# Kernel tuning notes

Measured on AMD Instinct MI355X. Metric: run time of the kernel, lower is better.

The kernel has to match this reference:

```python
import jax, jax.numpy as jnp
import numpy as np

B, IMG_ROWS, TSTEPS = 64, 32, 128
HID, CIN = 64, 512  # ncde hidden, ncde input dim = 32 * (IMG_ROWS//2)


def _linear(x, w, b):
    return x @ w.T + b


def _conv(x, w, b, pad):
    y = jax.lax.conv_general_dilated(x, w, (1, 1), [(pad, pad), (pad, pad)],
                                     dimension_numbers=('NCHW', 'OIHW', 'NCHW'))
    return y + b[None, :, None, None]


def _maxpool2(x):
    return jax.lax.reduce_window(x, -jnp.inf, jax.lax.max, (1, 1, 2, 2), (1, 1, 2, 2), 'VALID')


def _natural_cubic_coeffs(x):
    # x: [B, L, C], uniform knots t=0..L-1 (h=1). Natural cubic spline.
    L = x.shape[1]
    n = L - 2
    A = 4.0 * jnp.eye(n, dtype=x.dtype) + jnp.eye(n, k=1, dtype=x.dtype) + jnp.eye(n, k=-1, dtype=x.dtype)
    rhs = 6.0 * (x[:, 2:] - 2.0 * x[:, 1:-1] + x[:, :-2])  # [B, n, C]
    Mi = jnp.linalg.solve(A, rhs.transpose(1, 0, 2).reshape(n, -1))
    Mi = Mi.reshape(n, x.shape[0], x.shape[2]).transpose(1, 0, 2)
    M = jnp.pad(Mi, ((0, 0), (1, 1), (0, 0)))  # natural BCs: M0 = M_{L-1} = 0
    a = x[:, :-1]
    b = (x[:, 1:] - x[:, :-1]) - (2.0 * M[:, :-1] + M[:, 1:]) / 6.0
    c = M[:, :-1] / 2.0
    d = (M[:, 1:] - M[:, :-1]) / 6.0
    return a, b, c, d  # each [B, L-1, C]


def _forward(x, conv1_w, conv1_b, conv2_w, conv2_b, att_fc1_w, att_fc1_b,
             att_fc2_w, att_fc2_b, initial_w, initial_b, f1_w, f1_b,
             f2_w, f2_b, out_w, out_b):
    h = jax.nn.relu(_conv(x, conv1_w, conv1_b, pad=2))
    h = jax.nn.relu(_conv(h, conv2_w, conv2_b, pad=1))
    h = _maxpool2(h)  # [B,32,16,T/2]  (dropout is identity in eval)
    att = h.mean(axis=(2, 3))  # AdaptiveAvgPool2d(1)
    att = jax.nn.sigmoid(_linear(jax.nn.relu(_linear(att, att_fc1_w, att_fc1_b)), att_fc2_w, att_fc2_b))
    h = h * att[:, :, None, None]
    h = jnp.transpose(h, (0, 3, 1, 2))
    seq = h.reshape(h.shape[0], h.shape[1], -1)  # [B, L, 512]
    L = seq.shape[1]
    _, sb, sc, sd = _natural_cubic_coeffs(seq)

    z0 = _linear(seq[:, 0], initial_w, initial_b)  # spline.evaluate(t0) == seq[:,0]

    def cdefunc(z):
        u = jax.nn.relu(_linear(z, f1_w, f1_b))
        u = jnp.tanh(_linear(u, f2_w, f2_b))
        return u.reshape(z.shape[0], HID, CIN)

    def dXdt(t):
        seg = jnp.clip(jnp.floor(t).astype(jnp.int32), 0, L - 2)
        fr = t - seg.astype(t.dtype)
        return sb[:, seg] + 2.0 * sc[:, seg] * fr + 3.0 * sd[:, seg] * fr * fr

    def vf(t, z):
        return jnp.einsum('bhc,bc->bh', cdefunc(z), dXdt(t))

    dt = jnp.float32(0.5)
    nsteps = 2 * (L - 1)

    @jax.checkpoint
    def step(z, t):
        k1 = vf(t, z)
        k2 = vf(t + dt / 2, z + dt / 2 * k1)
        k3 = vf(t + dt / 2, z + dt / 2 * k2)
        k4 = vf(t + dt, z + dt * k3)
        return z + dt / 6.0 * (k1 + 2 * k2 + 2 * k3 + k4), None

    ts = jnp.arange(nsteps, dtype=jnp.float32) * dt
    zT, _ = jax.lax.scan(step, z0, ts)
    return _linear(zT, out_w, out_b)


def setup_inputs() -> dict:
    key = jax.random.key(0)
    ks = jax.random.split(key, 10)
    s = lambda k, shape, sc=0.05: (jax.random.normal(k, shape, jnp.float32) * sc)
    z = lambda n: jnp.zeros((n,), jnp.float32)
    return {
        'x': jax.random.normal(ks[0], (B, 1, IMG_ROWS, TSTEPS), jnp.float32),
        'conv1_w': s(ks[1], (32, 1, 5, 5)), 'conv1_b': z(32),
        'conv2_w': s(ks[2], (32, 32, 3, 3)), 'conv2_b': z(32),
        'att_fc1_w': s(ks[3], (4, 32)), 'att_fc1_b': z(4),
        'att_fc2_w': s(ks[4], (32, 4)), 'att_fc2_b': z(32),
        'initial_w': s(ks[5], (HID, CIN)), 'initial_b': z(HID),
        'f1_w': s(ks[6], (128, HID)), 'f1_b': z(128),
        'f2_w': s(ks[7], (CIN * HID, 128)), 'f2_b': z(CIN * HID),
        'out_w': s(ks[8], (2, HID)), 'out_b': z(2),
    }


def reference(x, conv1_w, conv1_b, conv2_w, conv2_b, att_fc1_w, att_fc1_b,
              att_fc2_w, att_fc2_b, initial_w, initial_b, f1_w, f1_b,
              f2_w, f2_b, out_w, out_b):
    return _forward(x, conv1_w, conv1_b, conv2_w, conv2_b, att_fc1_w, att_fc1_b,
                    att_fc2_w, att_fc2_b, initial_w, initial_b, f1_w, f1_b,
                    f2_w, f2_b, out_w, out_b)
```

## Files before the change

kernel.cpp:

```cpp
#include <hip/hip_runtime.h>
#include <hip/hip_bf16.h>
#include <stdint.h>

#define NSTEP 126
#define NEVAL 504
#define POISON 0xAAAAAAAAu

typedef __bf16 v8bf __attribute__((ext_vector_type(8)));
typedef float  v4f  __attribute__((ext_vector_type(4)));

__device__ __forceinline__ unsigned short f2bf(float x) {
  union { float f; uint32_t u; } v; v.f = x;
  uint32_t u = v.u;
  uint32_t r = (u + 0x7FFFu + ((u >> 16) & 1u)) >> 16;
  return (unsigned short)r;
}
__device__ __forceinline__ float bf2f(unsigned short b) {
  union { uint32_t u; float f; } v; v.u = ((uint32_t)b) << 16;
  return v.f;
}

__global__ void k_detect(const uint32_t* __restrict__ xw, int* flag) {
  __shared__ int cnt;
  if (threadIdx.x == 0) cnt = 0;
  __syncthreads();
  uint32_t w = xw[threadIdx.x];
  int e = (int)((w >> 7) & 0xFF);
  int good = ((e >= 100) && (e <= 144)) || ((w & 0xFFFFu) == 0u);
  atomicAdd(&cnt, good);
  __syncthreads();
  if (threadIdx.x == 0) *flag = (cnt >= 192) ? 1 : 0;
}

#define NCVT 15
struct CvtArgs {
  const void* src[NCVT];
  int dstoff[NCVT];
  int len[NCVT];
  int kind[NCVT];
  int total;
};
__global__ void k_convert(CvtArgs a, float* __restrict__ ws, const int* __restrict__ flag) {
  int f = *flag;
  for (int i = blockIdx.x*256 + threadIdx.x; i < a.total; i += gridDim.x*256) {
    int t = 0; int rem = i;
    while (rem >= a.len[t]) { rem -= a.len[t]; t++; }
    float v = f ? bf2f(((const unsigned short*)a.src[t])[rem])
                : ((const float*)a.src[t])[rem];
    int d;
    if (a.kind[t] == 1) { int h = rem >> 9, c = rem & 511; d = a.dstoff[t] + c*64 + h; }
    else if (a.kind[t] == 2) {
      int co = rem / 288, r2 = rem % 288;
      int ci = r2 / 9, tt = r2 % 9;
      d = a.dstoff[t] + (co >> 4)*4608 + (ci*16 + (co & 15))*9 + tt;
    }
    else d = a.dstoff[t] + rem;
    ws[d] = v;
  }
}

__global__ void k_wbf16(const void* __restrict__ w2src, const void* __restrict__ w1src,
                        unsigned short* __restrict__ w2bf, unsigned short* __restrict__ w1bf,
                        const int* __restrict__ flag) {
  int f = *flag;
  const long N2 = 4194304, N1 = 8192;
  for (long i = (long)blockIdx.x*256 + threadIdx.x; i < N2 + N1; i += (long)gridDim.x*256) {
    if (i < N2) w2bf[i] = f ? ((const unsigned short*)w2src)[i] : f2bf(((const float*)w2src)[i]);
    else { long j = i - N2; w1bf[j] = f ? ((const unsigned short*)w1src)[j] : f2bf(((const float*)w1src)[j]); }
  }
}

__global__ void k_conv1(const float* __restrict__ xf, const float* __restrict__ w,
                        const float* __restrict__ bias, float* __restrict__ h1) {
  int x = threadIdx.x;
  int y = blockIdx.x;
  int b = blockIdx.y;
  const float* xin = xf + (long)b*4096;
  float in[25];
  #pragma unroll
  for (int ky = 0; ky < 5; ky++) {
    int yy = y + ky - 2;
    #pragma unroll
    for (int kx = 0; kx < 5; kx++) {
      int xx = x + kx - 2;
      in[ky*5+kx] = (yy >= 0 && yy < 32 && xx >= 0 && xx < 128) ? xin[yy*128 + xx] : 0.f;
    }
  }
  for (int co = 0; co < 32; co++) {
    float acc = bias[co];
    #pragma unroll
    for (int t = 0; t < 25; t++) acc += in[t] * w[co*25 + t];
    h1[(((long)b*32 + co)*32 + y)*128 + x] = fmaxf(acc, 0.f);
  }
}

#define LD2 132
__global__ __launch_bounds__(256) void k_conv2(const float* __restrict__ h1, const float* __restrict__ w,
                                               const float* __restrict__ bias, float* __restrict__ h2) {
  __shared__ float s[32][3][LD2];
  int y = blockIdx.x, b = blockIdx.y;
  int tid = threadIdx.x;
  for (int i = tid; i < 32*3*LD2; i += 256) {
    int ci = i / (3*LD2);
    int r  = (i / LD2) % 3;
    int xx = i % LD2;
    int yy = y + r - 1, sx = xx - 1;
    float v = 0.f;
    if (yy >= 0 && yy < 32 && sx >= 0 && sx < 128) v = h1[(((long)b*32+ci)*32+yy)*128+sx];
    s[ci][r][xx] = v;
  }
  __syncthreads();
  int x = tid & 127;
  int half = __builtin_amdgcn_readfirstlane(tid >> 7);
  const float* wb = w + half*4608;
  float acc[16];
  #pragma unroll
  for (int i = 0; i < 16; i++) acc[i] = bias[half*16 + i];
  #pragma unroll 2
  for (int ci = 0; ci < 32; ci++) {
    float xv[9];
    #pragma unroll
    for (int r = 0; r < 3; r++)
      #pragma unroll
      for (int k = 0; k < 3; k++) xv[r*3+k] = s[ci][r][x + k];
    #pragma unroll
    for (int co = 0; co < 16; co++) {
      const float* wr = wb + (ci*16 + co)*9;
      #pragma unroll
      for (int t = 0; t < 9; t++) acc[co] += xv[t] * wr[t];
    }
  }
  #pragma unroll
  for (int co = 0; co < 16; co++)
    h2[(((long)b*32 + half*16 + co)*32 + y)*128 + x] = fmaxf(acc[co], 0.f);
}

__global__ void k_pool(const float* __restrict__ h2, float* __restrict__ pooled, float* __restrict__ attm) {
  int bc = blockIdx.x;
  const float* src = h2 + (long)bc*4096;
  float* dst = pooled + (long)bc*1024;
  float sum = 0.f;
  for (int i = threadIdx.x; i < 1024; i += 256) {
    int py = i >> 6, px = i & 63;
    const float* p = src + py*256 + px*2;
    float m = fmaxf(fmaxf(p[0], p[1]), fmaxf(p[128], p[129]));
    dst[i] = m;
    sum += m;
  }
  __shared__ float red[256];
  red[threadIdx.x] = sum;
  __syncthreads();
  for (int s2 = 128; s2 > 0; s2 >>= 1) {
    if (threadIdx.x < s2) red[threadIdx.x] += red[threadIdx.x + s2];
    __syncthreads();
  }
  if (threadIdx.x == 0) attm[bc] = red[0] * (1.f/1024.f);
}

__global__ void k_att(const float* __restrict__ attm, const float* __restrict__ w1, const float* __restrict__ b1,
                      const float* __restrict__ w2, const float* __restrict__ b2, float* __restrict__ atts) {
  int b = threadIdx.x;
  if (b < 64) {
    float hb[4];
    #pragma unroll
    for (int j = 0; j < 4; j++) {
      float s = b1[j];
      for (int i = 0; i < 32; i++) s += attm[b*32+i]*w1[j*32+i];
      hb[j] = fmaxf(s, 0.f);
    }
    for (int o = 0; o < 32; o++) {
      float s = b2[o];
      #pragma unroll
      for (int j = 0; j < 4; j++) s += hb[j]*w2[o*4+j];
      atts[b*32+o] = 1.f/(1.f + __expf(-s));
    }
  }
}

__global__ void k_seq(const float* __restrict__ pooled, const float* __restrict__ atts, float* __restrict__ seq) {
  for (int idx = blockIdx.x*256 + threadIdx.x; idx < 64*64*512; idx += gridDim.x*256) {
    int b = idx >> 15;
    int t = (idx >> 9) & 63;
    int fch = idx & 511;
    int c = fch >> 4, hh = fch & 15;
    seq[idx] = pooled[(((long)b*32 + c)*16 + hh)*64 + t] * atts[b*32 + c];
  }
}

__global__ __launch_bounds__(256, 1) void k_spline(const float* __restrict__ seq, float* __restrict__ sb,
                                                   float* __restrict__ sc, float* __restrict__ sd) {
  int id = blockIdx.x*256 + threadIdx.x;
  int b = id >> 9, f = id & 511;
  const float* xp = seq + (long)b*32768 + f;
  float xv[64];
  #pragma unroll
  for (int t = 0; t < 64; t++) xv[t] = xp[t*512];
  float cp[62], dp[62];
  float pc = 0.f, pd = 0.f;
  #pragma unroll
  for (int i = 0; i < 62; i++) {
    float rhs = 6.f*(xv[i+2] - 2.f*xv[i+1] + xv[i]);
    float inv = 1.f/(4.f - pc);
    pc = inv;
    pd = (rhs - pd)*inv;
    cp[i] = pc; dp[i] = pd;
  }
  #pragma unroll
  for (int i = 60; i >= 0; i--) dp[i] = dp[i] - cp[i]*dp[i+1];
  const float i6 = 1.f/6.f;
  #pragma unroll
  for (int t = 0; t < 63; t++) {
    float M0 = (t == 0)  ? 0.f : dp[t-1];
    float M1 = (t == 62) ? 0.f : dp[t];
    long o = ((long)b*63 + t)*512 + f;
    sb[o] = (xv[t+1] - xv[t]) - (2.f*M0 + M1)*i6;
    sc[o] = 0.5f*M0;
    sd[o] = (M1 - M0)*i6;
  }
}

__global__ void k_dxt(const float* __restrict__ sb, const float* __restrict__ sc,
                      const float* __restrict__ sd, float* __restrict__ dxt) {
  for (long i = (long)blockIdx.x*256 + threadIdx.x; i < (long)253*32768; i += (long)gridDim.x*256) {
    int m = (int)(i >> 15);
    int bf = (int)(i & 32767);
    int b = bf >> 9, c = bf & 511;
    int seg = m >> 2; if (seg > 62) seg = 62;
    float fr = 0.25f*(float)m - (float)seg;
    long o = ((long)b*63 + seg)*512 + c;
    dxt[i] = sb[o] + 2.f*fr*sc[o] + (3.f*fr*fr)*sd[o];
  }
}

__global__ void k_z0(const float* __restrict__ seq, const float* __restrict__ iwT,
                     const float* __restrict__ ib, float* __restrict__ z0) {
  __shared__ float s0[512];
  int b = blockIdx.x, h = threadIdx.x;
  for (int c = h; c < 512; c += 64) s0[c] = seq[(long)b*32768 + c];
  __syncthreads();
  float acc = ib[h];
  for (int c = 0; c < 512; c++) acc += s0[c]*iwT[c*64 + h];
  z0[b*64 + h] = acc;
}

__global__ __launch_bounds__(512, 2) void k_ode(
    const float* __restrict__ z0buf,
    const unsigned short* __restrict__ w2bf,
    const unsigned short* __restrict__ w1bf,
    const float* __restrict__ f1bias,
    const float* __restrict__ f2bias,
    const float* __restrict__ dxt,
    const float* __restrict__ outw,
    const float* __restrict__ outb,
    uint32_t* kpart,
    void* dout,
    const int* __restrict__ flag)
{
  __shared__ __align__(16) unsigned short zs[16*72];
  __shared__ __align__(16) unsigned short ub[16*136];
  __shared__ __align__(16) float dxs[16*524 + 10560];
  __shared__ float kred[128];

  int tid = threadIdx.x;
  int bl  = blockIdx.x;
  int hb  = bl >> 2;
  int bq  = bl & 3;
  int B0  = bq*16;
  int lane = tid & 63, wv = tid >> 6;
  int q = lane >> 4, ln = lane & 15;

  v8bf w2f[4][4];
  #pragma unroll
  for (int jt = 0; jt < 4; jt++)
    #pragma unroll
    for (int ks = 0; ks < 4; ks++) {
      long row = (long)hb*512 + wv*64 + jt*16 + ln;
      w2f[jt][ks] = *(const v8bf*)(w2bf + row*128 + ks*32 + q*8);
    }
  v8bf w1f[2];
  #pragma unroll
  for (int ks = 0; ks < 2; ks++)
    w1f[ks] = *(const v8bf*)(w1bf + (wv*16 + ln)*64 + ks*32 + q*8);
  float fb2[4][4];
  #pragma unroll
  for (int jt = 0; jt < 4; jt++)
    #pragma unroll
    for (int r = 0; r < 4; r++)
      fb2[jt][r] = f2bias[(long)hb*512 + wv*64 + jt*16 + q*4 + r];
  float fb1[4];
  #pragma unroll
  for (int r = 0; r < 4; r++)
    fb1[r] = f1bias[wv*16 + q*4 + r];

  int zbL = tid & 15;
  int hg  = tid >> 4;
  int h0  = hg*2;
  float z[2], zacc[2];
  #pragma unroll
  for (int i = 0; i < 2; i++) { z[i] = z0buf[(B0+zbL)*64 + h0 + i]; zacc[i] = 0.f; }

  const float dt6 = 0.5f/6.f;
  int e = 0;
  for (int step = 0; step < NSTEP; step++) {
    #pragma unroll 1
    for (int stage = 0; stage < 4; stage++, e++) {
      bool do_dx = (stage == 1) || (stage == 3) || (e == 0);
      int m = 2*step + ((stage + 1) >> 1);
      float4 dxr[4];
      if (do_dx) {
        #pragma unroll
        for (int i = 0; i < 4; i++) {
          int fi = i*512 + tid;
          int bb = fi >> 7, c4 = fi & 127;
          dxr[i] = *(const float4*)(dxt + (long)m*32768 + (B0+bb)*512 + c4*4);
        }
      }
      if (e > 0) {
        const uint32_t* kp = kpart + ((long)(e-1)*4 + bq)*1024;
        if (tid >= 64 && tid < 128) {
          const uint32_t* pp = kp + (tid - 64)*16;
          while (__hip_atomic_load(pp, __ATOMIC_RELAXED, __HIP_MEMORY_SCOPE_AGENT) == POISON)
            __builtin_amdgcn_s_sleep(1);
        }
        __syncthreads();
        float kv[2];
        #pragma unroll
        for (int i = 0; i < 2; i++) {
          const uint32_t* p = kp + (h0+i)*16 + zbL;
          uint32_t v = __hip_atomic_load(p, __ATOMIC_RELAXED, __HIP_MEMORY_SCOPE_AGENT);
          while (v == POISON) {
            __builtin_amdgcn_s_sleep(1);
            v = __hip_atomic_load(p, __ATOMIC_RELAXED, __HIP_MEMORY_SCOPE_AGENT);
          }
          kv[i] = __uint_as_float(v);
        }
        if (stage == 0) {
          uint32_t pk = 0;
          #pragma unroll
          for (int i = 0; i < 2; i++) {
            z[i] += dt6*(zacc[i] + kv[i]);
            zacc[i] = 0.f;
            pk |= ((uint32_t)f2bf(z[i])) << (16*i);
          }
          *(uint32_t*)(zs + zbL*72 + h0) = pk;
        } else {
          float wk = (stage == 1) ? 1.f : 2.f;
          float aa = (stage == 3) ? 0.5f : 0.25f;
          uint32_t pk = 0;
          #pragma unroll
          for (int i = 0; i < 2; i++) {
            zacc[i] += wk*kv[i];
            pk |= ((uint32_t)f2bf(z[i] + aa*kv[i])) << (16*i);
          }
          *(uint32_t*)(zs + zbL*72 + h0) = pk;
        }
      } else {
        uint32_t pk = ((uint32_t)f2bf(z[0])) | (((uint32_t)f2bf(z[1])) << 16);
        *(uint32_t*)(zs + zbL*72 + h0) = pk;
      }
      if (do_dx) {
        #pragma unroll
        for (int i = 0; i < 4; i++) {
          int fi = i*512 + tid;
          int bb = fi >> 7, c4 = fi & 127;
          *(float4*)(dxs + bb*524 + c4*4) = dxr[i];
        }
      }
      __syncthreads();
      v8bf zf[2];
      #pragma unroll
      for (int ks = 0; ks < 2; ks++)
        zf[ks] = *(const v8bf*)(zs + ln*72 + ks*32 + q*8);
      {
        v4f ua = (v4f){0.f, 0.f, 0.f, 0.f};
        #pragma unroll
        for (int ks = 0; ks < 2; ks++)
          ua = __builtin_amdgcn_mfma_f32_16x16x32_bf16(w1f[ks], zf[ks], ua, 0, 0, 0);
        ushort4 pk;
        pk.x = f2bf(fmaxf(ua[0] + fb1[0], 0.f));
        pk.y = f2bf(fmaxf(ua[1] + fb1[1], 0.f));
        pk.z = f2bf(fmaxf(ua[2] + fb1[2], 0.f));
        pk.w = f2bf(fmaxf(ua[3] + fb1[3], 0.f));
        *(ushort4*)(ub + ln*136 + wv*16 + q*4) = pk;
      }
      __syncthreads();
      v8bf uf[4];
      #pragma unroll
      for (int ks = 0; ks < 4; ks++)
        uf[ks] = *(const v8bf*)(ub + ln*136 + ks*32 + q*8);
      float ksum = 0.f;
      #pragma unroll
      for (int jt = 0; jt < 4; jt++) {
        v4f acc = (v4f){0.f, 0.f, 0.f, 0.f};
        #pragma unroll
        for (int ks = 0; ks < 4; ks++)
          acc = __builtin_amdgcn_mfma_f32_16x16x32_bf16(w2f[jt][ks], uf[ks], acc, 0, 0, 0);
        v4f dx4 = *(const v4f*)(dxs + ln*524 + wv*64 + jt*16 + q*4);
        #pragma unroll
        for (int r = 0; r < 4; r++) {
          float xv2 = acc[r] + fb2[jt][r];
          float ex = __expf(2.f*xv2);
          float th = 1.f - 2.f*__builtin_amdgcn_rcpf(ex + 1.f);
          ksum += th*dx4[r];
        }
      }
      ksum += __shfl_xor(ksum, 16, 64);
      ksum += __shfl_xor(ksum, 32, 64);
      if (lane < 16)
        kred[wv*16 + ln] = ksum;
      __syncthreads();
      if (tid < 16) {
        float v = 0.f;
        #pragma unroll
        for (int w = 0; w < 8; w++) v += kred[w*16 + tid];
        uint32_t uv = __float_as_uint(v);
        if (uv == POISON) uv ^= 1u;
        __hip_atomic_store(kpart + (((long)e*4 + bq)*64 + hb)*16 + tid, uv,
                           __ATOMIC_RELAXED, __HIP_MEMORY_SCOPE_AGENT);
      }
    }
  }
  if (hb == 0) {
    const uint32_t* kp = kpart + ((long)(NEVAL-1)*4 + bq)*1024;
    if (tid >= 64 && tid < 128) {
      const uint32_t* pp = kp + (tid - 64)*16;
      while (__hip_atomic_load(pp, __ATOMIC_RELAXED, __HIP_MEMORY_SCOPE_AGENT) == POISON)
        __builtin_amdgcn_s_sleep(1);
    }
    __syncthreads();
    {
      #pragma unroll
      for (int i = 0; i < 2; i++) {
        const uint32_t* p = kp + (h0+i)*16 + zbL;
        uint32_t v = __hip_atomic_load(p, __ATOMIC_RELAXED, __HIP_MEMORY_SCOPE_AGENT);
        while (v == POISON) {
          __builtin_amdgcn_s_sleep(1);
          v = __hip_atomic_load(p, __ATOMIC_RELAXED, __HIP_MEMORY_SCOPE_AGENT);
        }
        z[i] += dt6*(zacc[i] + __uint_as_float(v));
      }
    }
    float o0 = z[0]*outw[h0] + z[1]*outw[h0+1];
    float o1 = z[0]*outw[64+h0] + z[1]*outw[64+h0+1];
    __syncthreads();
    dxs[hg*32 + zbL*2 + 0] = o0;
    dxs[hg*32 + zbL*2 + 1] = o1;
    __syncthreads();
    if (tid < 32) {
      int bloc = tid >> 1, comp = tid & 1;
      float s = outb[comp];
      #pragma unroll
      for (int g = 0; g < 32; g++) s += dxs[g*32 + bloc*2 + comp];
      int b = B0 + bloc;
      if (*flag) ((unsigned short*)dout)[b*2 + comp] = f2bf(s);
      else       ((float*)dout)[b*2 + comp] = s;
    }
  }
}

extern "C" void kernel_launch(void* const* d_in, const int* in_sizes, int n_in,
                              void* d_out, int out_size, void* d_ws, size_t ws_size,
                              hipStream_t stream) {
  (void)in_sizes; (void)n_in; (void)out_size; (void)ws_size;
  float* ws = (float*)d_ws;
  size_t o = 0;
  auto alloc = [&](size_t n) { size_t r = o; o += (n + 63) & ~(size_t)63; return r; };
  size_t o_flag = alloc(64);
  size_t o_xf   = alloc(262144);
  size_t o_c1w  = alloc(800);
  size_t o_c1b  = alloc(32);
  size_t o_c2w  = alloc(9216);
  size_t o_c2b  = alloc(32);
  size_t o_a1w  = alloc(128);
  size_t o_a1b  = alloc(4);
  size_t o_a2w  = alloc(128);
  size_t o_a2b  = alloc(32);
  size_t o_iwT  = alloc(32768);
  size_t o_ib   = alloc(64);
  size_t o_f1b  = alloc(128);
  size_t o_f2b  = alloc(32768);
  size_t o_ow   = alloc(128);
  size_t o_ob   = alloc(2);
  size_t o_z0   = alloc(4096);
  size_t o_attm = alloc(2048);
  size_t o_atts = alloc(2048);
  size_t o_w1bf = alloc(4096);
  size_t o_w2bf = alloc(2097152);
  size_t o_h1   = alloc(8388608);
  size_t o_h2   = alloc(8388608);
  size_t o_kpart= alloc(4128768);
  size_t o_pool = o_h1;
  size_t o_seq  = o_h1 + 2097152;
  size_t o_dxt  = o_h1;
  size_t o_sb   = o_h2;
  size_t o_sc   = o_h2 + 2064384;
  size_t o_sd   = o_h2 + 4128768;

  int* flag = (int*)(ws + o_flag);

  hipLaunchKernelGGL(k_detect, dim3(1), dim3(256), 0, stream, (const uint32_t*)d_in[0], flag);

  CvtArgs ca;
  const int  si[NCVT]  = {0,1,2,3,4,5,6,7,8,9,10,12,14,15,16};
  const size_t dofs[NCVT] = {o_xf,o_c1w,o_c1b,o_c2w,o_c2b,o_a1w,o_a1b,o_a2w,o_a2b,o_iwT,o_ib,o_f1b,o_f2b,o_ow,o_ob};
  const int  ln[NCVT]  = {262144,800,32,9216,32,128,4,128,32,32768,64,128,32768,128,2};
  int tot = 0;
  for (int i = 0; i < NCVT; i++) {
    ca.src[i] = d_in[si[i]];
    ca.dstoff[i] = (int)dofs[i];
    ca.len[i] = ln[i];
    ca.kind[i] = (si[i] == 9) ? 1 : ((si[i] == 3) ? 2 : 0);
    tot += ln[i];
  }
  ca.total = tot;
  hipLaunchKernelGGL(k_convert, dim3(512), dim3(256), 0, stream, ca, ws, flag);
  hipLaunchKernelGGL(k_wbf16, dim3(2048), dim3(256), 0, stream, d_in[13], d_in[11],
                     (unsigned short*)(ws + o_w2bf), (unsigned short*)(ws + o_w1bf), flag);
  hipLaunchKernelGGL(k_conv1, dim3(32,64), dim3(128), 0, stream, ws+o_xf, ws+o_c1w, ws+o_c1b, ws+o_h1);
  hipLaunchKernelGGL(k_conv2, dim3(32,64), dim3(256), 0, stream, ws+o_h1, ws+o_c2w, ws+o_c2b, ws+o_h2);
  hipLaunchKernelGGL(k_pool, dim3(2048), dim3(256), 0, stream, ws+o_h2, ws+o_pool, ws+o_attm);
  hipLaunchKernelGGL(k_att, dim3(1), dim3(64), 0, stream, ws+o_attm, ws+o_a1w, ws+o_a1b, ws+o_a2w, ws+o_a2b, ws+o_atts);
  hipLaunchKernelGGL(k_seq, dim3(2048), dim3(256), 0, stream, ws+o_pool, ws+o_atts, ws+o_seq);
  hipLaunchKernelGGL(k_spline, dim3(128), dim3(256), 0, stream, ws+o_seq, ws+o_sb, ws+o_sc, ws+o_sd);
  hipLaunchKernelGGL(k_z0, dim3(64), dim3(64), 0, stream, ws+o_seq, ws+o_iwT, ws+o_ib, ws+o_z0);
  hipLaunchKernelGGL(k_dxt, dim3(4096), dim3(256), 0, stream, ws+o_sb, ws+o_sc, ws+o_sd, ws+o_dxt);

  hipLaunchKernelGGL(k_ode, dim3(256), dim3(512), 0, stream,
                     ws + o_z0,
                     (const unsigned short*)(ws + o_w2bf),
                     (const unsigned short*)(ws + o_w1bf),
                     ws + o_f1b, ws + o_f2b,
                     ws + o_dxt, ws + o_ow, ws + o_ob,
                     (uint32_t*)(ws + o_kpart),
                     d_out, (const int*)flag);
}
```

Measured before the change: 1.649 ms.

## Fuse spline dX/dt into spline kernel and stage k partials through LDS

The separate dX/dt kernel is removed: the spline kernel now writes dX/dt directly at the quarter-step sample points, so the sb/sc/sd intermediates never round-trip through global memory. In the ODE kernel, 256 threads poll the cross-block k partials in vectorised groups and stage them in LDS, replacing per-thread spinning atomic loads. Biases are folded into the MFMA accumulator initial values, bf16 packing uses the hardware pack-convert instruction, and the kred reduction layout is reordered. The added LDS buffer raises shared memory use per block, and the hardware conversion may round differently from the software round-to-nearest-even.

After: 1.704 ms. 1.03x slower.

```diff
diff --git a/kernel.cpp b/kernel.cpp
--- a/kernel.cpp
+++ b/kernel.cpp
@@ -18,6 +18,11 @@
 __device__ __forceinline__ float bf2f(unsigned short b) {
   union { uint32_t u; float f; } v; v.u = ((uint32_t)b) << 16;
   return v.f;
+}
+__device__ __forceinline__ uint32_t cvt_pk_bf16(float lo, float hi) {
+  uint32_t r;
+  asm("v_cvt_pk_bf16_f32 %0, %1, %2" : "=v"(r) : "v"(lo), "v"(hi));
+  return r;
 }
 
 __global__ void k_detect(const uint32_t* __restrict__ xw, int* flag) {
@@ -187,8 +192,8 @@
   }
 }
 
-__global__ __launch_bounds__(256, 1) void k_spline(const float* __restrict__ seq, float* __restrict__ sb,
-                                                   float* __restrict__ sc, float* __restrict__ sd) {
+__global__ __launch_bounds__(256, 1) void k_spline(const float* __restrict__ seq,
+                                                   float* __restrict__ dxt) {
   int id = blockIdx.x*256 + threadIdx.x;
   int b = id >> 9, f = id & 511;
   const float* xp = seq + (long)b*32768 + f;
@@ -208,27 +213,20 @@
   #pragma unroll
   for (int i = 60; i >= 0; i--) dp[i] = dp[i] - cp[i]*dp[i+1];
   const float i6 = 1.f/6.f;
+  float* op = dxt + (long)b*512 + f;
   #pragma unroll
   for (int t = 0; t < 63; t++) {
     float M0 = (t == 0)  ? 0.f : dp[t-1];
     float M1 = (t == 62) ? 0.f : dp[t];
-    long o = ((long)b*63 + t)*512 + f;
-    sb[o] = (xv[t+1] - xv[t]) - (2.f*M0 + M1)*i6;
-    sc[o] = 0.5f*M0;
-    sd[o] = (M1 - M0)*i6;
-  }
-}
-
-__global__ void k_dxt(const float* __restrict__ sb, const float* __restrict__ sc,
-                      const float* __restrict__ sd, float* __restrict__ dxt) {
-  for (long i = (long)blockIdx.x*256 + threadIdx.x; i < (long)253*32768; i += (long)gridDim.x*256) {
-    int m = (int)(i >> 15);
-    int bf = (int)(i & 32767);
-    int b = bf >> 9, c = bf & 511;
-    int seg = m >> 2; if (seg > 62) seg = 62;
-    float fr = 0.25f*(float)m - (float)seg;
-    long o = ((long)b*63 + seg)*512 + c;
-    dxt[i] = sb[o] + 2.f*fr*sc[o] + (3.f*fr*fr)*sd[o];
+    float sb = (xv[t+1] - xv[t]) - (2.f*M0 + M1)*i6;
+    float sc = 0.5f*M0;
+    float sd = (M1 - M0)*i6;
+    float* o = op + (long)(4*t)*32768;
+    o[0]      = sb;
+    o[32768]  = sb + 0.5f*sc + 0.1875f*sd;
+    o[65536]  = sb + sc + 0.75f*sd;
+    o[98304]  = sb + 1.5f*sc + 1.6875f*sd;
+    if (t == 62) o[131072] = sb + 2.f*sc + 3.f*sd;
   }
 }
 
@@ -258,7 +256,8 @@
 {
   __shared__ __align__(16) unsigned short zs[16*72];
   __shared__ __align__(16) unsigned short ub[16*136];
-  __shared__ __align__(16) float dxs[16*524 + 10560];
+  __shared__ __align__(16) float dxs[16*524 + 9600];
+  __shared__ __align__(16) uint32_t klds[1024];
   __shared__ float kred[128];
 
   int tid = threadIdx.x;
@@ -317,53 +316,56 @@
       }
       if (e > 0) {
         const uint32_t* kp = kpart + ((long)(e-1)*4 + bq)*1024;
-        if (tid >= 64 && tid < 128) {
-          const uint32_t* pp = kp + (tid - 64)*16;
-          while (__hip_atomic_load(pp, __ATOMIC_RELAXED, __HIP_MEMORY_SCOPE_AGENT) == POISON)
-            __builtin_amdgcn_s_sleep(1);
+        if (tid >= 64 && tid < 320) {
+          int pt = tid - 64;
+          const uint32_t* pp = kp + pt*4;
+          uint32_t v0 = __hip_atomic_load(pp+0, __ATOMIC_RELAXED, __HIP_MEMORY_SCOPE_AGENT);
+          uint32_t v1 = __hip_atomic_load(pp+1, __ATOMIC_RELAXED, __HIP_MEMORY_SCOPE_AGENT);
+          uint32_t v2 = __hip_atomic_load(pp+2, __ATOMIC_RELAXED, __HIP_MEMORY_SCOPE_AGENT);
+          uint32_t v3 = __hip_atomic_load(pp+3, __ATOMIC_RELAXED, __HIP_MEMORY_SCOPE_AGENT);
+          while (v0 == POISON) { __builtin_amdgcn_s_sleep(1);
+            v0 = __hip_atomic_load(pp+0, __ATOMIC_RELAXED, __HIP_MEMORY_SCOPE_AGENT); }
+          while (v1 == POISON) { __builtin_amdgcn_s_sleep(1);
+            v1 = __hip_atomic_load(pp+1, __ATOMIC_RELAXED, __HIP_MEMORY_SCOPE_AGENT); }
+          while (v2 == POISON) { __builtin_amdgcn_s_sleep(1);
+            v2 = __hip_atomic_load(pp+2, __ATOMIC_RELAXED, __HIP_MEMORY_SCOPE_AGENT); }
+          while (v3 == POISON) { __builtin_amdgcn_s_sleep(1);
+            v3 = __hip_atomic_load(pp+3, __ATOMIC_RELAXED, __HIP_MEMORY_SCOPE_AGENT); }
+          uint4 w4; w4.x = v0; w4.y = v1; w4.z = v2; w4.w = v3;
+          *(uint4*)(klds + pt*4) = w4;
         }
         __syncthreads();
-        float kv[2];
-        #pragma unroll
-        for (int i = 0; i < 2; i++) {
-          const uint32_t* p = kp + (h0+i)*16 + zbL;
-          uint32_t v = __hip_atomic_load(p, __ATOMIC_RELAXED, __HIP_MEMORY_SCOPE_AGENT);
-          while (v == POISON) {
-            __builtin_amdgcn_s_sleep(1);
-            v = __hip_atomic_load(p, __ATOMIC_RELAXED, __HIP_MEMORY_SCOPE_AGENT);
+        if (do_dx) {
+          #pragma unroll
+          for (int i = 0; i < 4; i++) {
+            int fi = i*512 + tid;
+            int bb = fi >> 7, c4 = fi & 127;
+            *(float4*)(dxs + bb*524 + c4*4) = dxr[i];
           }
-          kv[i] = __uint_as_float(v);
-        }
+        }
+        float kv0 = __uint_as_float(klds[h0*16 + zbL]);
+        float kv1 = __uint_as_float(klds[(h0+1)*16 + zbL]);
         if (stage == 0) {
-          uint32_t pk = 0;
-          #pragma unroll
-          for (int i = 0; i < 2; i++) {
-            z[i] += dt6*(zacc[i] + kv[i]);
-            zacc[i] = 0.f;
-            pk |= ((uint32_t)f2bf(z[i])) << (16*i);
-          }
-          *(uint32_t*)(zs + zbL*72 + h0) = pk;
+          z[0] += dt6*(zacc[0] + kv0);
+          z[1] += dt6*(zacc[1] + kv1);
+          zacc[0] = 0.f; zacc[1] = 0.f;
+          *(uint32_t*)(zs + zbL*72 + h0) = cvt_pk_bf16(z[0], z[1]);
         } else {
           float wk = (stage == 1) ? 1.f : 2.f;
           float aa = (stage == 3) ? 0.5f : 0.25f;
-          uint32_t pk = 0;
+          zacc[0] += wk*kv0;
+          zacc[1] += wk*kv1;
+          *(uint32_t*)(zs + zbL*72 + h0) = cvt_pk_bf16(z[0] + aa*kv0, z[1] + aa*kv1);
+        }
+      } else {
+        *(uint32_t*)(zs + zbL*72 + h0) = cvt_pk_bf16(z[0], z[1]);
+        if (do_dx) {
           #pragma unroll
-          for (int i = 0; i < 2; i++) {
-            zacc[i] += wk*kv[i];
-            pk |= ((uint32_t)f2bf(z[i] + aa*kv[i])) << (16*i);
+          for (int i = 0; i < 4; i++) {
+            int fi = i*512 + tid;
+            int bb = fi >> 7, c4 = fi & 127;
+            *(float4*)(dxs + bb*524 + c4*4) = dxr[i];
           }
-          *(uint32_t*)(zs + zbL*72 + h0) = pk;
-        }
-      } else {
-        uint32_t pk = ((uint32_t)f2bf(z[0])) | (((uint32_t)f2bf(z[1])) << 16);
-        *(uint32_t*)(zs + zbL*72 + h0) = pk;
-      }
-      if (do_dx) {
-        #pragma unroll
-        for (int i = 0; i < 4; i++) {
-          int fi = i*512 + tid;
-          int bb = fi >> 7, c4 = fi & 127;
-          *(float4*)(dxs + bb*524 + c4*4) = dxr[i];
         }
       }
       __syncthreads();
@@ -372,16 +374,14 @@
       for (int ks = 0; ks < 2; ks++)
         zf[ks] = *(const v8bf*)(zs + ln*72 + ks*32 + q*8);
       {
-        v4f ua = (v4f){0.f, 0.f, 0.f, 0.f};
+        v4f ua = (v4f){fb1[0], fb1[1], fb1[2], fb1[3]};
         #pragma unroll
         for (int ks = 0; ks < 2; ks++)
           ua = __builtin_amdgcn_mfma_f32_16x16x32_bf16(w1f[ks], zf[ks], ua, 0, 0, 0);
-        ushort4 pk;
-        pk.x = f2bf(fmaxf(ua[0] + fb1[0], 0.f));
-        pk.y = f2bf(fmaxf(ua[1] + fb1[1], 0.f));
-        pk.z = f2bf(fmaxf(ua[2] + fb1[2], 0.f));
-        pk.w = f2bf(fmaxf(ua[3] + fb1[3], 0.f));
-        *(ushort4*)(ub + ln*136 + wv*16 + q*4) = pk;
+        uint2 upk;
+        upk.x = cvt_pk_bf16(fmaxf(ua[0], 0.f), fmaxf(ua[1], 0.f));
+        upk.y = cvt_pk_bf16(fmaxf(ua[2], 0.f), fmaxf(ua[3], 0.f));
+        *(uint2*)(ub + ln*136 + wv*16 + q*4) = upk;
       }
       __syncthreads();
       v8bf uf[4];
@@ -391,14 +391,14 @@
       float ksum = 0.f;
       #pragma unroll
       for (int jt = 0; jt < 4; jt++) {
-        v4f acc = (v4f){0.f, 0.f, 0.f, 0.f};
+        v4f acc = (v4f){fb2[jt][0], fb2[jt][1], fb2[jt][2], fb2[jt][3]};
         #pragma unroll
         for (int ks = 0; ks < 4; ks++)
           acc = __builtin_amdgcn_mfma_f32_16x16x32_bf16(w2f[jt][ks], uf[ks], acc, 0, 0, 0);
         v4f dx4 = *(const v4f*)(dxs + ln*524 + wv*64 + jt*16 + q*4);
         #pragma unroll
         for (int r = 0; r < 4; r++) {
-          float xv2 = acc[r] + fb2[jt][r];
+          float xv2 = acc[r];
           float ex = __expf(2.f*xv2);
           float th = 1.f - 2.f*__builtin_amdgcn_rcpf(ex + 1.f);
           ksum += th*dx4[r];
@@ -407,12 +407,11 @@
       ksum += __shfl_xor(ksum, 16, 64);
       ksum += __shfl_xor(ksum, 32, 64);
       if (lane < 16)
-        kred[wv*16 + ln] = ksum;
+        kred[ln*8 + wv] = ksum;
       __syncthreads();
       if (tid < 16) {
-        float v = 0.f;
-        #pragma unroll
-        for (int w = 0; w < 8; w++) v += kred[w*16 + tid];
+        const float* kr = kred + tid*8;
+        float v = ((((((kr[0]+kr[1])+kr[2])+kr[3])+kr[4])+kr[5])+kr[6])+kr[7];
         uint32_t uv = __float_as_uint(v);
         if (uv == POISON) uv ^= 1u;
         __hip_atomic_store(kpart + (((long)e*4 + bq)*64 + hb)*16 + tid, uv,
@@ -491,10 +490,7 @@
   size_t o_kpart= alloc(4128768);
   size_t o_pool = o_h1;
   size_t o_seq  = o_h1 + 2097152;
-  size_t o_dxt  = o_h1;
-  size_t o_sb   = o_h2;
-  size_t o_sc   = o_h2 + 2064384;
-  size_t o_sd   = o_h2 + 4128768;
+  size_t o_dxt  = o_h2;
 
   int* flag = (int*)(ws + o_flag);
 
@@ -521,9 +517,8 @@
   hipLaunchKernelGGL(k_pool, dim3(2048), dim3(256), 0, stream, ws+o_h2, ws+o_pool, ws+o_attm);
   hipLaunchKernelGGL(k_att, dim3(1), dim3(64), 0, stream, ws+o_attm, ws+o_a1w, ws+o_a1b, ws+o_a2w, ws+o_a2b, ws+o_atts);
   hipLaunchKernelGGL(k_seq, dim3(2048), dim3(256), 0, stream, ws+o_pool, ws+o_atts, ws+o_seq);
-  hipLaunchKernelGGL(k_spline, dim3(128), dim3(256), 0, stream, ws+o_seq, ws+o_sb, ws+o_sc, ws+o_sd);
+  hipLaunchKernelGGL(k_spline, dim3(128), dim3(256), 0, stream, ws+o_seq, ws+o_dxt);
   hipLaunchKernelGGL(k_z0, dim3(64), dim3(64), 0, stream, ws+o_seq, ws+o_iwT, ws+o_ib, ws+o_z0);
-  hipLaunchKernelGGL(k_dxt, dim3(4096), dim3(256), 0, stream, ws+o_sb, ws+o_sc, ws+o_sd, ws+o_dxt);
 
   hipLaunchKernelGGL(k_ode, dim3(256), dim3(512), 0, stream,
                      ws + o_z0,
```
